# Kernel tuning notes

Hardware: AMD Instinct MI355X
Metric: run time of the kernel (lower is better)

The kernel has to match this reference:

```python
import jax, jax.numpy as jnp
import numpy as np

B, NC, PY, PX = 1, 2, 32, 32
DIM, HEADS = 1024, 16
IMAGE_H = IMAGE_W = 448
FREQ_BASE = 100.0


def _so3_exp(w):
    # w: (..., 3) axis-angle -> (..., 3, 3) rotation (Rodrigues)
    theta = jnp.maximum(jnp.linalg.norm(w, axis=-1, keepdims=True)[..., None], 1e-8)
    wx, wy, wz = w[..., 0], w[..., 1], w[..., 2]
    z = jnp.zeros_like(wx)
    K = jnp.stack([jnp.stack([z, -wz, wy], -1),
                   jnp.stack([wz, z, -wx], -1),
                   jnp.stack([-wy, wx, z], -1)], -2)
    A = jnp.sin(theta) / theta
    Bc = (1.0 - jnp.cos(theta)) / (theta * theta)
    return jnp.eye(3) + A * K + Bc * (K @ K)


def setup_inputs() -> dict:
    key = jax.random.key(0)
    ks = jax.random.split(key, 6)
    N = NC * PY * PX
    x = jax.random.normal(ks[0], (B, N, DIM), jnp.float32)
    # SE(3) camera extrinsics (world-to-camera)
    R = _so3_exp(0.2 * jax.random.normal(ks[1], (B, NC, 3), jnp.float32))
    t = 0.5 * jax.random.normal(ks[2], (B, NC, 3), jnp.float32)
    ext = jnp.zeros((B, NC, 4, 4), jnp.float32)
    ext = ext.at[..., :3, :3].set(R).at[..., :3, 3].set(t).at[..., 3, 3].set(1.0)
    f = 500.0
    Ks = jnp.zeros((B, NC, 3, 3), jnp.float32)
    Ks = (Ks.at[..., 0, 0].set(f).at[..., 1, 1].set(f)
            .at[..., 0, 2].set(IMAGE_W / 2.0).at[..., 1, 2].set(IMAGE_H / 2.0)
            .at[..., 2, 2].set(1.0))
    s = 1.0 / np.sqrt(DIM)
    qkv_w = s * jax.random.normal(ks[3], (3 * DIM, DIM), jnp.float32)
    proj_w = s * jax.random.normal(ks[4], (DIM, DIM), jnp.float32)
    proj_b = jnp.zeros((DIM,), jnp.float32)
    return dict(x=x, extrinsics=ext, Ks=Ks, qkv_w=qkv_w, proj_w=proj_w, proj_b=proj_b,
                image_h=IMAGE_H, image_w=IMAGE_W, patch_h=PY, patch_w=PX)


def _prope_attention(x, extrinsics, Ks, qkv_w, proj_w, proj_b,
                     image_h, image_w, patch_h, patch_w):
    Bb, N, C = x.shape
    H = HEADS
    D = C // H
    nc = extrinsics.shape[1]
    n_per = patch_h * patch_w  # tokens per camera

    # ---- QKV projection ----
    qkv = (x @ qkv_w.T).reshape(Bb, N, 3, H, D).transpose(0, 3, 2, 1, 4)  # B,H,3,N,D
    q, k, v = qkv[:, :, 0], qkv[:, :, 1], qkv[:, :, 2]

    # ---- per-camera normalized projection matrices P = K_norm(4x4) @ viewmat ----
    sx, sy = 2.0 / image_w, 2.0 / image_h  # pixel -> NDC-ish normalization
    Kn = jnp.zeros(Ks.shape[:-2] + (4, 4), x.dtype)
    Kn = (Kn.at[..., 0, 0].set(Ks[..., 0, 0] * sx)
            .at[..., 1, 1].set(Ks[..., 1, 1] * sy)
            .at[..., 0, 2].set(Ks[..., 0, 2] * sx - 1.0)
            .at[..., 1, 2].set(Ks[..., 1, 2] * sy - 1.0)
            .at[..., 2, 2].set(1.0).at[..., 3, 3].set(1.0))
    P = Kn @ extrinsics                      # (B, nc, 4, 4)
    P_inv = jnp.linalg.inv(P)

    def per_token(M):  # (B,nc,4,4) -> (B,N,4,4), broadcast camera over its tokens
        return jnp.repeat(M, n_per, axis=1)

    Mq = per_token(jnp.swapaxes(P_inv, -1, -2))  # P_i^{-T}
    Mk = per_token(P)                            # P_j
    Mo = per_token(P_inv)                        # P_i^{-1}

    # ---- channel split: half projective (blocks of 4), half 2D RoPE ----
    d_proj = D // 2
    d_rope = D - d_proj
    nf = d_rope // 4  # frequencies per axis (pairs of channels)
    freqs = FREQ_BASE ** (-jnp.arange(nf, dtype=x.dtype) / nf)
    ysg, xsg = jnp.meshgrid(jnp.arange(patch_h), jnp.arange(patch_w), indexing='ij')
    pos_x = jnp.tile(xsg.reshape(-1), nc).astype(x.dtype)  # (N,)
    pos_y = jnp.tile(ysg.reshape(-1), nc).astype(x.dtype)
    ang = jnp.concatenate([pos_x[:, None] * freqs, pos_y[:, None] * freqs], -1)  # (N, 2nf)
    cos, sin = jnp.cos(ang), jnp.sin(ang)

    def apply(t, M, sign):
        lead = t.shape[:-1]  # (B,H,N)
        tp = t[..., :d_proj].reshape(lead + (d_proj // 4, 4))
        tp = jnp.einsum('bnij,bhnkj->bhnki', M, tp).reshape(lead + (d_proj,))
        tr = t[..., d_proj:].reshape(lead + (2 * nf, 2))
        a, b = tr[..., 0], tr[..., 1]
        s = sign * sin
        tr = jnp.stack([a * cos - b * s, a * s + b * cos], -1).reshape(lead + (d_rope,))
        return jnp.concatenate([tp, tr], -1)

    q = apply(q, Mq, 1.0)
    k = apply(k, Mk, 1.0)
    v = apply(v, Mk, 1.0)

    # ---- SDPA ----
    scale = 1.0 / np.sqrt(D)
    attn = jax.nn.softmax(jnp.einsum('bhqd,bhkd->bhqk', q, k) * scale, axis=-1)
    out = jnp.einsum('bhqk,bhkd->bhqd', attn, v)

    # ---- inverse output transform ----
    out = apply(out, Mo, -1.0)
    out = out.transpose(0, 2, 1, 3).reshape(Bb, N, C)
    return out @ proj_w.T + proj_b


def reference(x, extrinsics, Ks, qkv_w, proj_w, proj_b, image_h, image_w, patch_h, patch_w):
    return _prope_attention(x, extrinsics, Ks, qkv_w, proj_w, proj_b,
                            image_h, image_w, patch_h, patch_w)
```

## Files before the change

kernel.cpp:

```cpp
#include <hip/hip_runtime.h>
#include <math.h>

#define N_TOK   2048
#define DIM     1024
#define HEADS   16
#define HD      64
#define NCAMS   2
#define NPER    1024
#define DPROJ   32
#define NF      8
#define KSPLIT  2

#define LOG2E   1.44269504088896340736f

typedef _Float16 half8  __attribute__((ext_vector_type(8)));
typedef _Float16 half4h __attribute__((ext_vector_type(4)));
typedef _Float16 half2h __attribute__((ext_vector_type(2)));
typedef __fp16   fp16x2 __attribute__((ext_vector_type(2)));
typedef float    floatx4 __attribute__((ext_vector_type(4)));

#define MATS_OFF  0
#define WPROJ_OFF 256
#define SCR_OFF   (WPROJ_OFF + 524288)
#define XF_OFF    (SCR_OFF)
#define WQKV_OFF  (SCR_OFF + 1048576)
#define OP_OFF    (SCR_OFF + 2621440)
#define ML_OFF    (SCR_OFF + 4718592)
#define Q_OFF     (SCR_OFF + 5767168)
#define K_OFF     (Q_OFF + 1048576)
#define V_OFF     (K_OFF + 1048576)

__device__ __forceinline__ void gl_lds16(const void* g, void* s) {
    __builtin_amdgcn_global_load_lds((const __attribute__((address_space(1))) void*)g,
                                     (__attribute__((address_space(3))) void*)s, 16, 0, 0);
}

__global__ __launch_bounds__(256) void cast_and_mats(const float* __restrict__ x,
                                                     const float* __restrict__ wqkv,
                                                     const float* __restrict__ wproj,
                                                     const float* __restrict__ ext,
                                                     const float* __restrict__ Ksm,
                                                     _Float16* __restrict__ xf,
                                                     _Float16* __restrict__ wqkvf,
                                                     _Float16* __restrict__ wprojf,
                                                     float* __restrict__ mats) {
    size_t i = ((size_t)blockIdx.x * 256 + threadIdx.x) * 8;
    const float* src; _Float16* dst; size_t off;
    if (i < (size_t)2*1024*1024)       { src = x;     dst = xf;     off = i; }
    else if (i < (size_t)5*1024*1024)  { src = wqkv;  dst = wqkvf;  off = i - (size_t)2*1024*1024; }
    else                               { src = wproj; dst = wprojf; off = i - (size_t)5*1024*1024; }
    float4 a = *(const float4*)(src + off);
    float4 b = *(const float4*)(src + off + 4);
    half8 h;
    h[0] = (_Float16)a.x; h[1] = (_Float16)a.y; h[2] = (_Float16)a.z; h[3] = (_Float16)a.w;
    h[4] = (_Float16)b.x; h[5] = (_Float16)b.y; h[6] = (_Float16)b.z; h[7] = (_Float16)b.w;
    *(half8*)(dst + off) = h;

    if (blockIdx.x == 0 && threadIdx.x < NCAMS) {
        const int c = threadIdx.x;
        const float sx = 2.0f / 448.0f, sy = 2.0f / 448.0f;
        const float* Kc = Ksm + c * 9;
        const float* E  = ext + c * 16;
        float Kn[16];
#pragma unroll
        for (int t = 0; t < 16; t++) Kn[t] = 0.0f;
        Kn[0]  = Kc[0] * sx;
        Kn[2]  = Kc[2] * sx - 1.0f;
        Kn[5]  = Kc[4] * sy;
        Kn[6]  = Kc[5] * sy - 1.0f;
        Kn[10] = 1.0f; Kn[15] = 1.0f;
        float P[16];
#pragma unroll
        for (int r = 0; r < 4; r++)
#pragma unroll
            for (int cc = 0; cc < 4; cc++) {
                float s = 0.0f;
#pragma unroll
                for (int k = 0; k < 4; k++) s += Kn[r*4+k] * E[k*4+cc];
                P[r*4+cc] = s;
            }
        float M[4][8];
        for (int r = 0; r < 4; r++)
            for (int cc = 0; cc < 4; cc++) { M[r][cc] = P[r*4+cc]; M[r][4+cc] = (r==cc) ? 1.0f : 0.0f; }
        for (int col = 0; col < 4; col++) {
            int piv = col;
            for (int r = col+1; r < 4; r++)
                if (fabsf(M[r][col]) > fabsf(M[piv][col])) piv = r;
            if (piv != col)
                for (int j = 0; j < 8; j++) { float tmp = M[col][j]; M[col][j] = M[piv][j]; M[piv][j] = tmp; }
            float d = 1.0f / M[col][col];
            for (int j = 0; j < 8; j++) M[col][j] *= d;
            for (int r = 0; r < 4; r++) {
                if (r == col) continue;
                float f = M[r][col];
                for (int j = 0; j < 8; j++) M[r][j] -= f * M[col][j];
            }
        }
        float Pi[16];
        for (int r = 0; r < 4; r++)
            for (int cc = 0; cc < 4; cc++) Pi[r*4+cc] = M[r][4+cc];
        float* o = mats + c * 48;
        for (int r = 0; r < 4; r++)
            for (int cc = 0; cc < 4; cc++) o[r*4+cc] = Pi[cc*4+r];
        for (int t = 0; t < 16; t++) o[16+t] = P[t];
        for (int t = 0; t < 16; t++) o[32+t] = Pi[t];
    }
}

__global__ __launch_bounds__(256) void gemm_qkv_fused(const _Float16* __restrict__ A,
                                                      const _Float16* __restrict__ Bw,
                                                      const float* __restrict__ mats,
                                                      _Float16* __restrict__ Qf,
                                                      _Float16* __restrict__ Kf,
                                                      _Float16* __restrict__ Vtf) {
    const int Kd = DIM;
    __shared__ _Float16 As[2][64 * 32];
    __shared__ _Float16 Bs[2][128 * 32];
    const int tid  = threadIdx.x;
    const int w    = tid >> 6, lane = tid & 63;
    const int ql   = lane & 15, quad = lane >> 4;
    const int lr   = lane >> 2, lc = lane & 3;
    const int row0 = blockIdx.y * 64, col0 = blockIdx.x * 128;

    floatx4 acc[4][2];
#pragma unroll
    for (int mt = 0; mt < 4; mt++)
#pragma unroll
        for (int nt = 0; nt < 2; nt++) acc[mt][nt] = (floatx4){0.f, 0.f, 0.f, 0.f};

    const _Float16* Ab  = A  + (size_t)(row0 + w * 16 + lr) * Kd + lc * 8;
    const _Float16* Bb0 = Bw + (size_t)(col0 + w * 32 + lr) * Kd + lc * 8;
    const _Float16* Bb1 = Bw + (size_t)(col0 + w * 32 + 16 + lr) * Kd + lc * 8;

    gl_lds16(Ab,  &As[0][(w * 16) * 32]);
    gl_lds16(Bb0, &Bs[0][(w * 32) * 32]);
    gl_lds16(Bb1, &Bs[0][(w * 32 + 16) * 32]);

    const int nIter = Kd >> 5;
    for (int i = 0; i < nIter; i++) {
        __syncthreads();
        if (i + 1 < nIter) {
            const int k0 = (i + 1) << 5;
            const int nb = (i + 1) & 1;
            gl_lds16(Ab + k0,  &As[nb][(w * 16) * 32]);
            gl_lds16(Bb0 + k0, &Bs[nb][(w * 32) * 32]);
            gl_lds16(Bb1 + k0, &Bs[nb][(w * 32 + 16) * 32]);
        }
        const int cur = i & 1;
        half8 af[4], bf[2];
#pragma unroll
        for (int mt = 0; mt < 4; mt++)
            af[mt] = *(const half8*)&As[cur][(mt * 16 + ql) * 32 + quad * 8];
#pragma unroll
        for (int nt = 0; nt < 2; nt++)
            bf[nt] = *(const half8*)&Bs[cur][(w * 32 + nt * 16 + ql) * 32 + quad * 8];
#pragma unroll
        for (int mt = 0; mt < 4; mt++)
#pragma unroll
            for (int nt = 0; nt < 2; nt++)
                acc[mt][nt] = __builtin_amdgcn_mfma_f32_16x16x32_f16(af[mt], bf[nt], acc[mt][nt], 0, 0, 0);
    }

    const int s   = col0 >> 10;
    const int cam = row0 >> 10;
    const float* Amat = mats + cam * 48 + (s == 0 ? 0 : 16);
    const int i4 = (ql & 3) * 4;
    const float A0 = Amat[i4+0], A1 = Amat[i4+1], A2 = Amat[i4+2], A3 = Amat[i4+3];
    const int g = lane & ~3;
    const float sc = (s == 0) ? 0.125f * LOG2E : 1.0f;

#pragma unroll
    for (int nt = 0; nt < 2; nt++) {
        const int cb = col0 + w * 32 + nt * 16;
        const int dbase = cb & 63;
        const int d = dbase + ql;
        const int h = (cb >> 6) & 15;
        float out[4][4];
        if (dbase < 32) {
#pragma unroll
            for (int mt = 0; mt < 4; mt++)
#pragma unroll
                for (int r = 0; r < 4; r++) {
                    const float v  = acc[mt][nt][r];
                    const float t0 = __shfl(v, g + 0, 64);
                    const float t1 = __shfl(v, g + 1, 64);
                    const float t2 = __shfl(v, g + 2, 64);
                    const float t3 = __shfl(v, g + 3, 64);
                    out[mt][r] = A0*t0 + A1*t1 + A2*t2 + A3*t3;
                }
        } else {
            const int pt = (d - 32) >> 1;
            const float fr = __expf(-0.5756462732485114f * (float)(pt & 7));
            const bool usex = (pt < NF);
#pragma unroll
            for (int mt = 0; mt < 4; mt++)
#pragma unroll
                for (int r = 0; r < 4; r++) {
                    const float v = acc[mt][nt][r];
                    const float other = __shfl_xor(v, 1, 64);
                    const int n = row0 + mt * 16 + quad * 4 + r;
                    const int p = n & (NPER - 1);
                    const float pos = (float)(usex ? (p & 31) : (p >> 5));
                    float sn, cs; __sincosf(pos * fr, &sn, &cs);
                    const float sgn = (d & 1) ? sn : -sn;
                    out[mt][r] = v * cs + other * sgn;
                }
        }
        if (s < 2) {
            _Float16* dst = (s == 0) ? Qf : Kf;
#pragma unroll
            for (int mt = 0; mt < 4; mt++)
#pragma unroll
                for (int r = 0; r < 4; r++) {
                    const int n = row0 + mt * 16 + quad * 4 + r;
                    dst[((size_t)h * N_TOK + n) * HD + d] = (_Float16)(out[mt][r] * sc);
                }
        } else {
#pragma unroll
            for (int mt = 0; mt < 4; mt++) {
                half4h o4;
#pragma unroll
                for (int r = 0; r < 4; r++) o4[r] = (_Float16)out[mt][r];
                const int n0 = row0 + mt * 16 + quad * 4;
                *(half4h*)&Vtf[((size_t)h * HD + d) * N_TOK + n0] = o4;
            }
        }
    }
}

#define PLD 68
__global__ __launch_bounds__(256) void attn_mfma(const _Float16* __restrict__ Qh,
                                                 const _Float16* __restrict__ Kh,
                                                 const _Float16* __restrict__ Vt,
                                                 _Float16* __restrict__ OP,
                                                 float* __restrict__ ML) {
    __shared__ _Float16 sK[64 * 64];
    __shared__ _Float16 sV[64 * 64];
    __shared__ _Float16 P_lds[4][16][PLD];
    const int w    = threadIdx.x >> 6;
    const int lane = threadIdx.x & 63;
    const int b  = blockIdx.x;
    const int ks = b >> 9;
    const int hh = (b >> 5) & 15;
    const int qb = b & 31;
    const int ql = lane & 15, quad = lane >> 4;
    const int q0 = qb * 64 + w * 16;

    const int srow = lane >> 3;
    const int schk = (lane & 7) ^ srow;
    const int c0 = ((quad ^ (ql & 7)) << 3);
    const int c1 = c0 ^ 32;

    const _Float16* Qp = Qh + ((size_t)hh * N_TOK + q0 + ql) * HD;
    const half8 qf0 = *(const half8*)(Qp + quad * 8);
    const half8 qf1 = *(const half8*)(Qp + 32 + quad * 8);

    const _Float16* Kb = Kh + (size_t)hh * N_TOK * HD;
    const _Float16* Vb = Vt + (size_t)hh * HD * N_TOK;

    floatx4 O[4];
#pragma unroll
    for (int mt = 0; mt < 4; mt++) O[mt] = (floatx4){0.f, 0.f, 0.f, 0.f};
    float m = -1e30f, l = 0.0f;

    const int kstart = ks * (N_TOK / KSPLIT);
    const int nIter  = (N_TOK / KSPLIT) / 64;

    for (int i = 0; i < nIter; i++) {
        const int kb = kstart + i * 64;
#pragma unroll
        for (int j = 0; j < 2; j++) {
            const int r0 = w * 16 + j * 8;
            gl_lds16(Kb + (size_t)(kb + r0 + srow) * HD + schk * 8, &sK[r0 * 64]);
            gl_lds16(Vb + (size_t)(r0 + srow) * N_TOK + kb + schk * 8, &sV[r0 * 64]);
        }
        __syncthreads();
        floatx4 s[4];
#pragma unroll
        for (int kt = 0; kt < 4; kt++) {
            const int rb = (kt * 16 + ql) * 64;
            half8 ka0 = *(const half8*)&sK[rb + c0];
            half8 ka1 = *(const half8*)&sK[rb + c1];
            floatx4 acc = (floatx4){0.f, 0.f, 0.f, 0.f};
            acc = __builtin_amdgcn_mfma_f32_16x16x32_f16(ka0, qf0, acc, 0, 0, 0);
            acc = __builtin_amdgcn_mfma_f32_16x16x32_f16(ka1, qf1, acc, 0, 0, 0);
            s[kt] = acc;
        }
        float bm = -1e30f;
#pragma unroll
        for (int kt = 0; kt < 4; kt++)
#pragma unroll
            for (int r = 0; r < 4; r++) bm = fmaxf(bm, s[kt][r]);
        bm = fmaxf(bm, __shfl_xor(bm, 16, 64));
        bm = fmaxf(bm, __shfl_xor(bm, 32, 64));
        const float mnew = fmaxf(m, bm);
        if (__ballot(bm > m)) {
            const float alpha = exp2f(m - mnew);
            l *= alpha;
#pragma unroll
            for (int mt = 0; mt < 4; mt++)
#pragma unroll
                for (int r = 0; r < 4; r++) O[mt][r] *= alpha;
        }
        m = mnew;
        float p[4][4];
        float ps = 0.0f;
#pragma unroll
        for (int kt = 0; kt < 4; kt++)
#pragma unroll
            for (int r = 0; r < 4; r++) { p[kt][r] = exp2f(s[kt][r] - mnew); ps += p[kt][r]; }
        l += ps;
#pragma unroll
        for (int kt = 0; kt < 4; kt++) {
            union { fp16x2 h; half2h v; } u01, u23;
            u01.h = __builtin_amdgcn_cvt_pkrtz(p[kt][0], p[kt][1]);
            u23.h = __builtin_amdgcn_cvt_pkrtz(p[kt][2], p[kt][3]);
            *(half2h*)&P_lds[w][ql][kt * 16 + quad * 4]     = u01.v;
            *(half2h*)&P_lds[w][ql][kt * 16 + quad * 4 + 2] = u23.v;
        }
        union { half8 v8; half4h v4[2]; } pu0, pu1;
        pu0.v4[0] = *(const half4h*)&P_lds[w][ql][quad * 8];
        pu0.v4[1] = *(const half4h*)&P_lds[w][ql][quad * 8 + 4];
        pu1.v4[0] = *(const half4h*)&P_lds[w][ql][32 + quad * 8];
        pu1.v4[1] = *(const half4h*)&P_lds[w][ql][32 + quad * 8 + 4];
#pragma unroll
        for (int mt = 0; mt < 4; mt++) {
            const int rb = (mt * 16 + ql) * 64;
            half8 va0 = *(const half8*)&sV[rb + c0];
            half8 va1 = *(const half8*)&sV[rb + c1];
            O[mt] = __builtin_amdgcn_mfma_f32_16x16x32_f16(va0, pu0.v8, O[mt], 0, 0, 0);
            O[mt] = __builtin_amdgcn_mfma_f32_16x16x32_f16(va1, pu1.v8, O[mt], 0, 0, 0);
        }
        __syncthreads();
    }
    l += __shfl_xor(l, 16, 64);
    l += __shfl_xor(l, 32, 64);
    const float rl = 1.0f / l;
    _Float16* Op = OP + (((size_t)(ks * HEADS + hh)) * N_TOK + q0 + ql) * HD;
#pragma unroll
    for (int mt = 0; mt < 4; mt++) {
        half4h o4;
#pragma unroll
        for (int r = 0; r < 4; r++) o4[r] = (_Float16)(O[mt][r] * rl);
        *(half4h*)&Op[mt * 16 + quad * 4] = o4;
    }
    if (quad == 0) {
        float2 mlv = {m, l};
        *(float2*)&ML[(((size_t)(ks * HEADS + hh)) * N_TOK + q0 + ql) * 2] = mlv;
    }
}

__global__ __launch_bounds__(256) void gemm_proj_fused(const _Float16* __restrict__ OP,
                                                       const float* __restrict__ ML,
                                                       const float* __restrict__ mats,
                                                       const _Float16* __restrict__ Bw,
                                                       const float* __restrict__ bias,
                                                       float* __restrict__ C) {
    const int Kd = DIM, Nn = DIM;
    __shared__ _Float16 As[2][64 * 32];
    __shared__ _Float16 Bs[2][128 * 32];
    const int tid  = threadIdx.x;
    const int w    = tid >> 6, lane = tid & 63;
    const int ql   = lane & 15, quad = lane >> 4;
    const int lr   = lane >> 2, lc = lane & 3;
    const int row0 = blockIdx.y * 64, col0 = blockIdx.x * 128;

    const int n   = row0 + w * 16 + lr;
    const int cam = row0 >> 10;
    const float* Ao = mats + cam * 48 + 32;
    const int p = n & (NPER - 1);
    const float px = (float)(p & 31), py = (float)(p >> 5);

    floatx4 acc[4][2];
#pragma unroll
    for (int mt = 0; mt < 4; mt++)
#pragma unroll
        for (int nt = 0; nt < 2; nt++) acc[mt][nt] = (floatx4){0.f, 0.f, 0.f, 0.f};

    const _Float16* Bb0 = Bw + (size_t)(col0 + w * 32 + lr) * Kd + lc * 8;
    const _Float16* Bb1 = Bw + (size_t)(col0 + w * 32 + 16 + lr) * Kd + lc * 8;

    auto stageA = [&](int k0, _Float16* dstLds) {
        const int h = k0 >> 6;
        const int d = (k0 & 32) + lc * 8;
        float2 ml0 = *(const float2*)&ML[(((size_t)h) * N_TOK + n) * 2];
        float2 ml1 = *(const float2*)&ML[(((size_t)(HEADS + h)) * N_TOK + n) * 2];
        half8 op0 = *(const half8*)&OP[(((size_t)h) * N_TOK + n) * HD + d];
        half8 op1 = *(const half8*)&OP[(((size_t)(HEADS + h)) * N_TOK + n) * HD + d];
        const float mstar = fmaxf(ml0.x, ml1.x);
        const float w0 = exp2f(ml0.x - mstar) * ml0.y;
        const float w1 = exp2f(ml1.x - mstar) * ml1.y;
        const float rW = 1.0f / (w0 + w1);
        const float wa = w0 * rW, wb = w1 * rW;
        float t[8], r[8];
#pragma unroll
        for (int j = 0; j < 8; j++) t[j] = wa * (float)op0[j] + wb * (float)op1[j];
        if (d < 32) {
#pragma unroll
            for (int g = 0; g < 2; g++)
#pragma unroll
                for (int i = 0; i < 4; i++)
                    r[g*4+i] = Ao[i*4+0]*t[g*4+0] + Ao[i*4+1]*t[g*4+1]
                             + Ao[i*4+2]*t[g*4+2] + Ao[i*4+3]*t[g*4+3];
        } else {
#pragma unroll
            for (int pp = 0; pp < 4; pp++) {
                const int pt = lc * 4 + pp;
                const float fr = __expf(-0.5756462732485114f * (float)(pt & 7));
                const float ang = (pt < NF ? px : py) * fr;
                float sn, cs; __sincosf(ang, &sn, &cs);
                const float a = t[pp*2], b = t[pp*2+1];
                r[pp*2]   = a * cs + b * sn;
                r[pp*2+1] = -a * sn + b * cs;
            }
        }
        union { half8 v8; fp16x2 h2[4]; } o;
#pragma unroll
        for (int pp = 0; pp < 4; pp++)
            o.h2[pp] = __builtin_amdgcn_cvt_pkrtz(r[pp*2], r[pp*2+1]);
        *(half8*)&dstLds[(w * 16 + lr) * 32 + lc * 8] = o.v8;
    };

    stageA(0, As[0]);
    gl_lds16(Bb0, &Bs[0][(w * 32) * 32]);
    gl_lds16(Bb1, &Bs[0][(w * 32 + 16) * 32]);

    const int nIter = Kd >> 5;
    for (int i = 0; i < nIter; i++) {
        __syncthreads();
        if (i + 1 < nIter) {
            const int k0 = (i + 1) << 5;
            const int nb = (i + 1) & 1;
            stageA(k0, As[nb]);
            gl_lds16(Bb0 + k0, &Bs[nb][(w * 32) * 32]);
            gl_lds16(Bb1 + k0, &Bs[nb][(w * 32 + 16) * 32]);
        }
        const int cur = i & 1;
        half8 af[4], bf[2];
#pragma unroll
        for (int mt = 0; mt < 4; mt++)
            af[mt] = *(const half8*)&As[cur][(mt * 16 + ql) * 32 + quad * 8];
#pragma unroll
        for (int nt = 0; nt < 2; nt++)
            bf[nt] = *(const half8*)&Bs[cur][(w * 32 + nt * 16 + ql) * 32 + quad * 8];
#pragma unroll
        for (int mt = 0; mt < 4; mt++)
#pragma unroll
            for (int nt = 0; nt < 2; nt++)
                acc[mt][nt] = __builtin_amdgcn_mfma_f32_16x16x32_f16(af[mt], bf[nt], acc[mt][nt], 0, 0, 0);
    }

#pragma unroll
    for (int nt = 0; nt < 2; nt++) {
        const int col = col0 + w * 32 + nt * 16 + ql;
        const float bb = bias[col];
#pragma unroll
        for (int mt = 0; mt < 4; mt++) {
            const int row = row0 + mt * 16 + quad * 4;
#pragma unroll
            for (int r = 0; r < 4; r++)
                C[(size_t)(row + r) * Nn + col] = acc[mt][nt][r] + bb;
        }
    }
}

extern "C" void kernel_launch(void* const* d_in, const int* in_sizes, int n_in,
                              void* d_out, int out_size, void* d_ws, size_t ws_size,
                              hipStream_t stream) {
    const float* x      = (const float*)d_in[0];
    const float* ext    = (const float*)d_in[1];
    const float* Ks     = (const float*)d_in[2];
    const float* qkv_w  = (const float*)d_in[3];
    const float* proj_w = (const float*)d_in[4];
    const float* proj_b = (const float*)d_in[5];
    float* out = (float*)d_out;

    float* ws   = (float*)d_ws;
    float* mats = ws + MATS_OFF;
    _Float16* Wprojf = (_Float16*)(ws + WPROJ_OFF);
    _Float16* Xf     = (_Float16*)(ws + XF_OFF);
    _Float16* Wqkvf  = (_Float16*)(ws + WQKV_OFF);
    _Float16* OP     = (_Float16*)(ws + OP_OFF);
    float*    ML     = ws + ML_OFF;
    _Float16* Qf  = (_Float16*)(ws + Q_OFF);
    _Float16* Kf  = (_Float16*)(ws + K_OFF);
    _Float16* Vtf = (_Float16*)(ws + V_OFF);

    cast_and_mats<<<3072, 256, 0, stream>>>(x, qkv_w, proj_w, ext, Ks,
                                            Xf, Wqkvf, Wprojf, mats);

    gemm_qkv_fused<<<dim3(3*DIM/128, N_TOK/64), 256, 0, stream>>>(
        Xf, Wqkvf, mats, Qf, Kf, Vtf);

    attn_mfma<<<KSPLIT * HEADS * (N_TOK / 64), 256, 0, stream>>>(Qf, Kf, Vtf, OP, ML);

    gemm_proj_fused<<<dim3(DIM/128, N_TOK/64), 256, 0, stream>>>(
        OP, ML, mats, Wprojf, proj_b, out);
}
```

Before: 184.6 us.

## Process two 16-row query tiles per wave in attention to reuse K/V tiles

New measurement: 188.8 us. 1.02x slower.

```diff
diff --git a/kernel.cpp b/kernel.cpp
--- a/kernel.cpp
+++ b/kernel.cpp
@@ -236,32 +236,35 @@
                                                  float* __restrict__ ML) {
     __shared__ _Float16 sK[64 * 64];
     __shared__ _Float16 sV[64 * 64];
-    __shared__ _Float16 P_lds[4][16][PLD];
+    __shared__ _Float16 P_lds[4][32][PLD];
     const int w    = threadIdx.x >> 6;
     const int lane = threadIdx.x & 63;
     const int b  = blockIdx.x;
-    const int ks = b >> 9;
-    const int hh = (b >> 5) & 15;
-    const int qb = b & 31;
+    const int ks = b >> 8;
+    const int hh = (b >> 4) & 15;
+    const int qb = b & 15;
     const int ql = lane & 15, quad = lane >> 4;
-    const int q0 = qb * 64 + w * 16;
+    const int q0 = qb * 128 + w * 32;
 
     const int srow = lane >> 3;
     const int schk = (lane & 7) ^ srow;
     const int c0 = ((quad ^ (ql & 7)) << 3);
     const int c1 = c0 ^ 32;
 
-    const _Float16* Qp = Qh + ((size_t)hh * N_TOK + q0 + ql) * HD;
-    const half8 qf0 = *(const half8*)(Qp + quad * 8);
-    const half8 qf1 = *(const half8*)(Qp + 32 + quad * 8);
+    const _Float16* QpA = Qh + ((size_t)hh * N_TOK + q0 + ql) * HD;
+    const _Float16* QpB = QpA + 16 * HD;
+    const half8 qa0 = *(const half8*)(QpA + quad * 8);
+    const half8 qa1 = *(const half8*)(QpA + 32 + quad * 8);
+    const half8 qb0 = *(const half8*)(QpB + quad * 8);
+    const half8 qb1 = *(const half8*)(QpB + 32 + quad * 8);
 
     const _Float16* Kb = Kh + (size_t)hh * N_TOK * HD;
     const _Float16* Vb = Vt + (size_t)hh * HD * N_TOK;
 
-    floatx4 O[4];
-#pragma unroll
-    for (int mt = 0; mt < 4; mt++) O[mt] = (floatx4){0.f, 0.f, 0.f, 0.f};
-    float m = -1e30f, l = 0.0f;
+    floatx4 OA[4], OB[4];
+#pragma unroll
+    for (int mt = 0; mt < 4; mt++) { OA[mt] = (floatx4){0.f,0.f,0.f,0.f}; OB[mt] = (floatx4){0.f,0.f,0.f,0.f}; }
+    float mA = -1e30f, lA = 0.0f, mB = -1e30f, lB = 0.0f;
 
     const int kstart = ks * (N_TOK / KSPLIT);
     const int nIter  = (N_TOK / KSPLIT) / 64;
@@ -275,78 +278,126 @@
             gl_lds16(Vb + (size_t)(r0 + srow) * N_TOK + kb + schk * 8, &sV[r0 * 64]);
         }
         __syncthreads();
-        floatx4 s[4];
+        floatx4 sA[4], sB[4];
 #pragma unroll
         for (int kt = 0; kt < 4; kt++) {
             const int rb = (kt * 16 + ql) * 64;
             half8 ka0 = *(const half8*)&sK[rb + c0];
             half8 ka1 = *(const half8*)&sK[rb + c1];
-            floatx4 acc = (floatx4){0.f, 0.f, 0.f, 0.f};
-            acc = __builtin_amdgcn_mfma_f32_16x16x32_f16(ka0, qf0, acc, 0, 0, 0);
-            acc = __builtin_amdgcn_mfma_f32_16x16x32_f16(ka1, qf1, acc, 0, 0, 0);
-            s[kt] = acc;
-        }
-        float bm = -1e30f;
-#pragma unroll
-        for (int kt = 0; kt < 4; kt++)
-#pragma unroll
-            for (int r = 0; r < 4; r++) bm = fmaxf(bm, s[kt][r]);
-        bm = fmaxf(bm, __shfl_xor(bm, 16, 64));
-        bm = fmaxf(bm, __shfl_xor(bm, 32, 64));
-        const float mnew = fmaxf(m, bm);
-        if (__ballot(bm > m)) {
-            const float alpha = exp2f(m - mnew);
-            l *= alpha;
-#pragma unroll
-            for (int mt = 0; mt < 4; mt++)
-#pragma unroll
-                for (int r = 0; r < 4; r++) O[mt][r] *= alpha;
-        }
-        m = mnew;
-        float p[4][4];
-        float ps = 0.0f;
-#pragma unroll
-        for (int kt = 0; kt < 4; kt++)
-#pragma unroll
-            for (int r = 0; r < 4; r++) { p[kt][r] = exp2f(s[kt][r] - mnew); ps += p[kt][r]; }
-        l += ps;
-#pragma unroll
-        for (int kt = 0; kt < 4; kt++) {
-            union { fp16x2 h; half2h v; } u01, u23;
-            u01.h = __builtin_amdgcn_cvt_pkrtz(p[kt][0], p[kt][1]);
-            u23.h = __builtin_amdgcn_cvt_pkrtz(p[kt][2], p[kt][3]);
-            *(half2h*)&P_lds[w][ql][kt * 16 + quad * 4]     = u01.v;
-            *(half2h*)&P_lds[w][ql][kt * 16 + quad * 4 + 2] = u23.v;
-        }
-        union { half8 v8; half4h v4[2]; } pu0, pu1;
-        pu0.v4[0] = *(const half4h*)&P_lds[w][ql][quad * 8];
-        pu0.v4[1] = *(const half4h*)&P_lds[w][ql][quad * 8 + 4];
-        pu1.v4[0] = *(const half4h*)&P_lds[w][ql][32 + quad * 8];
-        pu1.v4[1] = *(const half4h*)&P_lds[w][ql][32 + quad * 8 + 4];
+            floatx4 aA = (floatx4){0.f,0.f,0.f,0.f};
+            aA = __builtin_amdgcn_mfma_f32_16x16x32_f16(ka0, qa0, aA, 0, 0, 0);
+            aA = __builtin_amdgcn_mfma_f32_16x16x32_f16(ka1, qa1, aA, 0, 0, 0);
+            sA[kt] = aA;
+            floatx4 aB = (floatx4){0.f,0.f,0.f,0.f};
+            aB = __builtin_amdgcn_mfma_f32_16x16x32_f16(ka0, qb0, aB, 0, 0, 0);
+            aB = __builtin_amdgcn_mfma_f32_16x16x32_f16(ka1, qb1, aB, 0, 0, 0);
+            sB[kt] = aB;
+        }
+        {
+            float bm = -1e30f;
+#pragma unroll
+            for (int kt = 0; kt < 4; kt++)
+#pragma unroll
+                for (int r = 0; r < 4; r++) bm = fmaxf(bm, sA[kt][r]);
+            bm = fmaxf(bm, __shfl_xor(bm, 16, 64));
+            bm = fmaxf(bm, __shfl_xor(bm, 32, 64));
+            const float mnew = fmaxf(mA, bm);
+            if (__ballot(bm > mA)) {
+                const float alpha = exp2f(mA - mnew);
+                lA *= alpha;
+#pragma unroll
+                for (int mt = 0; mt < 4; mt++)
+#pragma unroll
+                    for (int r = 0; r < 4; r++) OA[mt][r] *= alpha;
+            }
+            mA = mnew;
+            float ps = 0.0f;
+#pragma unroll
+            for (int kt = 0; kt < 4; kt++) {
+                float p0 = exp2f(sA[kt][0] - mnew), p1 = exp2f(sA[kt][1] - mnew);
+                float p2 = exp2f(sA[kt][2] - mnew), p3 = exp2f(sA[kt][3] - mnew);
+                ps += p0 + p1 + p2 + p3;
+                union { fp16x2 h; half2h v; } u01, u23;
+                u01.h = __builtin_amdgcn_cvt_pkrtz(p0, p1);
+                u23.h = __builtin_amdgcn_cvt_pkrtz(p2, p3);
+                *(half2h*)&P_lds[w][ql][kt * 16 + quad * 4]     = u01.v;
+                *(half2h*)&P_lds[w][ql][kt * 16 + quad * 4 + 2] = u23.v;
+            }
+            lA += ps;
+        }
+        {
+            float bm = -1e30f;
+#pragma unroll
+            for (int kt = 0; kt < 4; kt++)
+#pragma unroll
+                for (int r = 0; r < 4; r++) bm = fmaxf(bm, sB[kt][r]);
+            bm = fmaxf(bm, __shfl_xor(bm, 16, 64));
+            bm = fmaxf(bm, __shfl_xor(bm, 32, 64));
+            const float mnew = fmaxf(mB, bm);
+            if (__ballot(bm > mB)) {
+                const float alpha = exp2f(mB - mnew);
+                lB *= alpha;
+#pragma unroll
+                for (int mt = 0; mt < 4; mt++)
+#pragma unroll
+                    for (int r = 0; r < 4; r++) OB[mt][r] *= alpha;
+            }
+            mB = mnew;
+            float ps = 0.0f;
+#pragma unroll
+            for (int kt = 0; kt < 4; kt++) {
+                float p0 = exp2f(sB[kt][0] - mnew), p1 = exp2f(sB[kt][1] - mnew);
+                float p2 = exp2f(sB[kt][2] - mnew), p3 = exp2f(sB[kt][3] - mnew);
+                ps += p0 + p1 + p2 + p3;
+                union { fp16x2 h; half2h v; } u01, u23;
+                u01.h = __builtin_amdgcn_cvt_pkrtz(p0, p1);
+                u23.h = __builtin_amdgcn_cvt_pkrtz(p2, p3);
+                *(half2h*)&P_lds[w][16 + ql][kt * 16 + quad * 4]     = u01.v;
+                *(half2h*)&P_lds[w][16 + ql][kt * 16 + quad * 4 + 2] = u23.v;
+            }
+            lB += ps;
+        }
+        union { half8 v8; half4h v4[2]; } pA0, pA1, pB0, pB1;
+        pA0.v4[0] = *(const half4h*)&P_lds[w][ql][quad * 8];
+        pA0.v4[1] = *(const half4h*)&P_lds[w][ql][quad * 8 + 4];
+        pA1.v4[0] = *(const half4h*)&P_lds[w][ql][32 + quad * 8];
+        pA1.v4[1] = *(const half4h*)&P_lds[w][ql][32 + quad * 8 + 4];
+        pB0.v4[0] = *(const half4h*)&P_lds[w][16 + ql][quad * 8];
+        pB0.v4[1] = *(const half4h*)&P_lds[w][16 + ql][quad * 8 + 4];
+        pB1.v4[0] = *(const half4h*)&P_lds[w][16 + ql][32 + quad * 8];
+        pB1.v4[1] = *(const half4h*)&P_lds[w][16 + ql][32 + quad * 8 + 4];
 #pragma unroll
         for (int mt = 0; mt < 4; mt++) {
             const int rb = (mt * 16 + ql) * 64;
             half8 va0 = *(const half8*)&sV[rb + c0];
             half8 va1 = *(const half8*)&sV[rb + c1];
-            O[mt] = __builtin_amdgcn_mfma_f32_16x16x32_f16(va0, pu0.v8, O[mt], 0, 0, 0);
-            O[mt] = __builtin_amdgcn_mfma_f32_16x16x32_f16(va1, pu1.v8, O[mt], 0, 0, 0);
+            OA[mt] = __builtin_amdgcn_mfma_f32_16x16x32_f16(va0, pA0.v8, OA[mt], 0, 0, 0);
+            OA[mt] = __builtin_amdgcn_mfma_f32_16x16x32_f16(va1, pA1.v8, OA[mt], 0, 0, 0);
+            OB[mt] = __builtin_amdgcn_mfma_f32_16x16x32_f16(va0, pB0.v8, OB[mt], 0, 0, 0);
+            OB[mt] = __builtin_amdgcn_mfma_f32_16x16x32_f16(va1, pB1.v8, OB[mt], 0, 0, 0);
         }
         __syncthreads();
     }
-    l += __shfl_xor(l, 16, 64);
-    l += __shfl_xor(l, 32, 64);
-    const float rl = 1.0f / l;
-    _Float16* Op = OP + (((size_t)(ks * HEADS + hh)) * N_TOK + q0 + ql) * HD;
+    lA += __shfl_xor(lA, 16, 64);
+    lA += __shfl_xor(lA, 32, 64);
+    lB += __shfl_xor(lB, 16, 64);
+    lB += __shfl_xor(lB, 32, 64);
+    const float rlA = 1.0f / lA, rlB = 1.0f / lB;
+    _Float16* OpA = OP + (((size_t)(ks * HEADS + hh)) * N_TOK + q0 + ql) * HD;
+    _Float16* OpB = OpA + 16 * HD;
 #pragma unroll
     for (int mt = 0; mt < 4; mt++) {
-        half4h o4;
-#pragma unroll
-        for (int r = 0; r < 4; r++) o4[r] = (_Float16)(O[mt][r] * rl);
-        *(half4h*)&Op[mt * 16 + quad * 4] = o4;
+        half4h oa, ob;
+#pragma unroll
+        for (int r = 0; r < 4; r++) { oa[r] = (_Float16)(OA[mt][r] * rlA); ob[r] = (_Float16)(OB[mt][r] * rlB); }
+        *(half4h*)&OpA[mt * 16 + quad * 4] = oa;
+        *(half4h*)&OpB[mt * 16 + quad * 4] = ob;
     }
     if (quad == 0) {
-        float2 mlv = {m, l};
-        *(float2*)&ML[(((size_t)(ks * HEADS + hh)) * N_TOK + q0 + ql) * 2] = mlv;
+        float2 mlvA = {mA, lA};
+        float2 mlvB = {mB, lB};
+        *(float2*)&ML[(((size_t)(ks * HEADS + hh)) * N_TOK + q0 + ql) * 2] = mlvA;
+        *(float2*)&ML[(((size_t)(ks * HEADS + hh)) * N_TOK + q0 + 16 + ql) * 2] = mlvB;
     }
 }
 
@@ -492,7 +543,7 @@
     gemm_qkv_fused<<<dim3(3*DIM/128, N_TOK/64), 256, 0, stream>>>(
         Xf, Wqkvf, mats, Qf, Kf, Vtf);
 
-    attn_mfma<<<KSPLIT * HEADS * (N_TOK / 64), 256, 0, stream>>>(Qf, Kf, Vtf, OP, ML);
+    attn_mfma<<<KSPLIT * HEADS * (N_TOK / 128), 256, 0, stream>>>(Qf, Kf, Vtf, OP, ML);
 
     gemm_proj_fused<<<dim3(DIM/128, N_TOK/64), 256, 0, stream>>>(
         OP, ML, mats, Wprojf, proj_b, out);
```
